# Kernel optimization log

Measured on AMD Instinct MI355X. Metric: run time of the kernel, lower is better.

The kernel has to match this reference:

```python
import jax, jax.numpy as jnp
import numpy as np

B, V = 2048, 64          # batch of polygons, vertices per polygon
D = 2 * V                # data_dim (flattened 2D coords)
HID, TDIM, NL = 256, 128, 4
NH_HID, FPH = 4, 64      # hidden heads, per-head features (hidden_dim//4)
NIN = 2 + 4 + TDIM       # coords + pos_enc(4) + time emb


def _gat_layer(h, src, tgt, W, a_src, a_tgt, b, skip, concat, act, N):
    # gordicaleksa pytorch-GAT GATLayer (imp3), dropout=0
    NH, FOUT = a_src.shape
    proj = (h @ W).reshape(N, NH, FOUT)                       # (N,NH,FOUT)
    s_src = (proj * a_src).sum(-1)                            # (N,NH)
    s_tgt = (proj * a_tgt).sum(-1)
    e = jax.nn.leaky_relu(s_src[src] + s_tgt[tgt], negative_slope=0.2)  # (E,NH)
    m = jax.ops.segment_max(e, tgt, num_segments=N)           # stable segment softmax
    ex = jnp.exp(e - m[tgt])
    denom = jax.ops.segment_sum(ex, tgt, num_segments=N)
    alpha = ex / (denom[tgt] + 1e-16)                         # (E,NH)
    out = jax.ops.segment_sum(proj[src] * alpha[:, :, None], tgt, num_segments=N)
    if skip is None:                                          # FIN == FOUT -> direct residual
        out = out + h[:, None, :]
    else:
        out = out + (h @ skip).reshape(N, NH, FOUT)
    out = out.reshape(N, NH * FOUT) if concat else out.mean(axis=1)
    out = out + b
    return jax.nn.elu(out) if act else out


def _forward(x, t, tW, tb, layers, h1W, h1b, h2W, h2b):
    Bsz, Dd = x.shape
    Vn = Dd // 2
    N = Bsz * Vn
    coords = x.reshape(N, 2)
    graph_index = jnp.repeat(jnp.arange(Bsz), Vn)
    node_index = jnp.tile(jnp.arange(Vn), Bsz)
    # SinusoidalPosEmb(TDIM) + Linear + SiLU
    half = TDIM // 2
    freqs = jnp.exp(-jnp.log(10000.0) * jnp.arange(half, dtype=jnp.float32) / (half - 1))
    te = t.astype(jnp.float32)[:, None] * freqs[None, :]
    temb = jnp.concatenate([jnp.sin(te), jnp.cos(te)], axis=1)
    temb = jax.nn.silu(temb @ tW + tb)
    # cycle positional features
    phase = node_index.astype(jnp.float32) * (2.0 * jnp.pi / Vn)
    pos = jnp.stack([jnp.sin(phase), jnp.cos(phase), jnp.sin(2.0 * phase), jnp.cos(2.0 * phase)], axis=1)
    h = jnp.concatenate([coords, pos, temb[graph_index]], axis=1)  # (N, NIN)
    # cycle edge_index: src=[self,self,self], tgt=[next,prev,self]
    base = graph_index * Vn
    slf = jnp.arange(N)
    nxt = base + jnp.remainder(node_index + 1, Vn)
    prv = base + jnp.remainder(node_index - 1, Vn)
    src = jnp.concatenate([slf, slf, slf])
    tgt = jnp.concatenate([nxt, prv, slf])
    for i, (W, a_s, a_t, b, skip) in enumerate(layers):
        last = (i == len(layers) - 1)
        h = _gat_layer(h, src, tgt, W, a_s, a_t, b, skip, concat=not last, act=not last, N=N)
    h = jax.nn.silu(h @ h1W + h1b)
    noise = h @ h2W + h2b                                     # (N, 2)
    return noise.reshape(Bsz, Dd)


def setup_inputs() -> dict:
    key = jax.random.key(0)
    ks = iter(jax.random.split(key, 48))
    def nrm(shape, s=0.05):
        return (jax.random.normal(next(ks), shape, jnp.float32) * s)
    inp = {}
    inp["x"] = jax.random.normal(next(ks), (B, D), jnp.float32)
    inp["t"] = jax.random.randint(next(ks), (B,), 0, 1000)
    inp["tW"] = nrm((TDIM, TDIM)); inp["tb"] = jnp.zeros((TDIM,), jnp.float32)
    fins = [NIN, NH_HID * FPH, NH_HID * FPH, NH_HID * FPH]
    fouts = [FPH, FPH, FPH, HID]
    nhs = [NH_HID, NH_HID, NH_HID, 1]
    for i in range(NL):
        inp[f"W{i}"] = nrm((fins[i], nhs[i] * fouts[i]))
        inp[f"asrc{i}"] = nrm((nhs[i], fouts[i]))
        inp[f"atgt{i}"] = nrm((nhs[i], fouts[i]))
        inp[f"b{i}"] = jnp.zeros((nhs[i] * fouts[i] if i < NL - 1 else fouts[i],), jnp.float32)
    for i in range(NL - 1):  # last layer: FIN==FOUT -> identity skip
        inp[f"skip{i}"] = nrm((fins[i], nhs[i] * fouts[i]))
    inp["h1W"] = nrm((HID, HID)); inp["h1b"] = jnp.zeros((HID,), jnp.float32)
    inp["h2W"] = nrm((HID, 2)); inp["h2b"] = jnp.zeros((2,), jnp.float32)
    return inp


def reference(x, t, tW, tb,
              W0, asrc0, atgt0, b0, skip0,
              W1, asrc1, atgt1, b1, skip1,
              W2, asrc2, atgt2, b2, skip2,
              W3, asrc3, atgt3, b3,
              h1W, h1b, h2W, h2b):
    layers = [(W0, asrc0, atgt0, b0, skip0),
              (W1, asrc1, atgt1, b1, skip1),
              (W2, asrc2, atgt2, b2, skip2),
              (W3, asrc3, atgt3, b3, None)]
    return _forward(x, t, tW, tb, layers, h1W, h1b, h2W, h2b)
```

## Files before the change

### kernel.cpp

```cpp
#include <hip/hip_runtime.h>
#include <hip/hip_bf16.h>

#define VN    64
#define KPAD  264

typedef __bf16 bf16x8 __attribute__((ext_vector_type(8)));
typedef float  f32x4  __attribute__((ext_vector_type(4)));

#define OFF_W0   0
#define OFF_SK0  40960
#define OFF_W1   81920
#define OFF_SK1  147456
#define OFF_W2   212992
#define OFF_SK2  278528
#define OFF_W3   344064
#define OFF_H1W  409600
#define OFF_END  475136

__global__ void pack_all(const float* __restrict__ W0s, const float* __restrict__ sk0s,
                         const float* __restrict__ W1s, const float* __restrict__ sk1s,
                         const float* __restrict__ W2s, const float* __restrict__ sk2s,
                         const float* __restrict__ W3s, const float* __restrict__ h1Ws,
                         const float* __restrict__ h2W, float* __restrict__ h2wt,
                         __bf16* __restrict__ wp)
{
  int blk = blockIdx.x;
  if (blk >= 1856) {
    int idx = (blk - 1856) * 256 + threadIdx.x;
    int c = idx >> 8, k = idx & 255;
    h2wt[idx] = h2W[k * 2 + c];
    return;
  }
  const float* src; int fin, dstoff, rel;
  if (blk < 320) {
    if (blk < 160) { src = W0s;  dstoff = OFF_W0;  rel = blk; }
    else           { src = sk0s; dstoff = OFF_SK0; rel = blk - 160; }
    fin = 134;
  } else {
    int r = (blk - 320) >> 8;
    rel = (blk - 320) & 255;
    const float* srcs[6] = {W1s, sk1s, W2s, sk2s, W3s, h1Ws};
    const int    offs[6] = {OFF_W1, OFF_SK1, OFF_W2, OFF_SK2, OFF_W3, OFF_H1W};
    src = srcs[r]; dstoff = offs[r]; fin = 256;
  }
  int idx = rel * 256 + threadIdx.x;
  int rr = idx & 7, n = (idx >> 3) & 255, c = idx >> 11;
  int k = c * 8 + rr;
  float v = (k < fin) ? src[k * 256 + n] : 0.0f;
  wp[dstoff + idx] = (__bf16)v;
}

__global__ void temb_kernel(const int* __restrict__ t, const float* __restrict__ tW,
                            const float* __restrict__ tb, float* __restrict__ d_temb)
{
  __shared__ float se[128];
  int b = blockIdx.x, tid = threadIdx.x;
  int fi = tid & 63;
  float fr = expf(-logf(10000.0f) * (float)fi / 63.0f);
  float te = (float)t[b] * fr;
  se[tid] = (tid < 64) ? sinf(te) : cosf(te);
  __syncthreads();
  float a = tb[tid];
  for (int k = 0; k < 128; k++)
    a = fmaf(se[k], tW[k * 128 + tid], a);
  d_temb[b * 128 + tid] = a / (1.0f + expf(-a));
}

template<int KS>
__device__ __forceinline__ void mfma_mm(const __bf16* __restrict__ Bp,
                                        f32x4 acc[4][4],
                                        const __bf16* __restrict__ shA,
                                        int l, int q, int colbase8)
{
#pragma unroll
  for (int s = 0; s < KS; s++) {
    bf16x8 af[4], bfr[4];
#pragma unroll
    for (int rt = 0; rt < 4; rt++)
      af[rt] = *(const bf16x8*)(shA + (rt * 16 + l) * KPAD + s * 32 + q * 8);
#pragma unroll
    for (int ct = 0; ct < 4; ct++)
      bfr[ct] = *(const bf16x8*)(Bp + (s * 4 + q) * 2048 + colbase8 + ct * 128);
#pragma unroll
    for (int rt = 0; rt < 4; rt++)
#pragma unroll
      for (int ct = 0; ct < 4; ct++)
        acc[rt][ct] = __builtin_amdgcn_mfma_f32_16x16x32_bf16(af[rt], bfr[ct], acc[rt][ct], 0, 0, 0);
  }
}

template<int KS>
__device__ __forceinline__ void mfma_dual(const __bf16* __restrict__ Bw,
                                          const __bf16* __restrict__ Bk,
                                          f32x4 accW[4][4], f32x4 accK[4][4],
                                          const __bf16* __restrict__ shA,
                                          int l, int q, int colbase8)
{
#pragma unroll
  for (int s = 0; s < KS; s++) {
    bf16x8 af[4], bw[4], bk[4];
#pragma unroll
    for (int rt = 0; rt < 4; rt++)
      af[rt] = *(const bf16x8*)(shA + (rt * 16 + l) * KPAD + s * 32 + q * 8);
#pragma unroll
    for (int ct = 0; ct < 4; ct++) {
      bw[ct] = *(const bf16x8*)(Bw + (s * 4 + q) * 2048 + colbase8 + ct * 128);
      bk[ct] = *(const bf16x8*)(Bk + (s * 4 + q) * 2048 + colbase8 + ct * 128);
    }
#pragma unroll
    for (int rt = 0; rt < 4; rt++)
#pragma unroll
      for (int ct = 0; ct < 4; ct++) {
        accW[rt][ct] = __builtin_amdgcn_mfma_f32_16x16x32_bf16(af[rt], bw[ct], accW[rt][ct], 0, 0, 0);
        accK[rt][ct] = __builtin_amdgcn_mfma_f32_16x16x32_bf16(af[rt], bk[ct], accK[rt][ct], 0, 0, 0);
      }
  }
}

__global__ __launch_bounds__(256, 2)
void gat_poly_kernel(const float* __restrict__ x,
                     const float* __restrict__ as0, const float* __restrict__ at0, const float* __restrict__ b0,
                     const float* __restrict__ as1, const float* __restrict__ at1, const float* __restrict__ b1,
                     const float* __restrict__ as2, const float* __restrict__ at2, const float* __restrict__ b2,
                     const float* __restrict__ as3, const float* __restrict__ at3, const float* __restrict__ b3,
                     const float* __restrict__ h1b, const float* __restrict__ h2b,
                     const __bf16* __restrict__ WP,
                     const float* __restrict__ h2wt,
                     const float* __restrict__ d_temb,
                     float* __restrict__ out)
{
  __shared__ __bf16 sh_hb[VN * KPAD];
  __shared__ float  sh_temb[128];
  __shared__ float  sh_ssp[VN * 4];
  __shared__ float  sh_stp[VN * 4];
  __shared__ float  sh_al[VN][3];

  const int b    = blockIdx.x;
  const int tid  = threadIdx.x;
  const int w    = tid >> 6;
  const int lane = tid & 63;
  const int l    = lane & 15;
  const int q    = lane >> 4;
  const int cb   = w * 64;
  const int colbase8 = (cb + l) * 8;
  const int lup  = (lane + 16) & 63;
  const int ldn  = (lane + 48) & 63;

  if (tid < 128) sh_temb[tid] = d_temb[b * 128 + tid];
  __syncthreads();

  for (int idx = tid; idx < VN * 160; idx += 256) {
    int n = idx / 160, k = idx - n * 160;
    float v = 0.0f;
    if (k < 2) {
      v = x[b * 128 + 2 * n + k];
    } else if (k < 6) {
      float ph  = (float)n * 0.09817477042468103f;
      float arg = (k < 4) ? ph : 2.0f * ph;
      v = ((k & 1) == 0) ? sinf(arg) : cosf(arg);
    } else if (k < 134) {
      v = sh_temb[k - 6];
    }
    sh_hb[n * KPAD + k] = (__bf16)v;
  }
  __syncthreads();

  const int WOFFS[3]  = {OFF_W0, OFF_W1, OFF_W2};
  const int SOFFS[3]  = {OFF_SK0, OFF_SK1, OFF_SK2};
  const float* Asr[3] = {as0, as1, as2};
  const float* Atg[3] = {at0, at1, at2};
  const float* Bs[3]  = {b0, b1, b2};

  for (int li = 0; li < 3; li++) {
    f32x4 accP[4][4], accS[4][4];
#pragma unroll
    for (int rt = 0; rt < 4; rt++)
#pragma unroll
      for (int ct = 0; ct < 4; ct++) { accP[rt][ct] = (f32x4)0.0f; accS[rt][ct] = (f32x4)0.0f; }

    if (li == 0) mfma_dual<5>(WP + OFF_W0,   WP + OFF_SK0,   accP, accS, sh_hb, l, q, colbase8);
    else         mfma_dual<8>(WP + WOFFS[li], WP + SOFFS[li], accP, accS, sh_hb, l, q, colbase8);

    float ca[4], ta[4];
#pragma unroll
    for (int ct = 0; ct < 4; ct++) {
      ca[ct] = Asr[li][cb + ct * 16 + l];
      ta[ct] = Atg[li][cb + ct * 16 + l];
    }
    float ssA[4][4], stA[4][4];
#pragma unroll
    for (int rt = 0; rt < 4; rt++)
#pragma unroll
      for (int reg = 0; reg < 4; reg++) {
        float ss = accP[rt][0][reg] * ca[0] + accP[rt][1][reg] * ca[1]
                 + accP[rt][2][reg] * ca[2] + accP[rt][3][reg] * ca[3];
        float st = accP[rt][0][reg] * ta[0] + accP[rt][1][reg] * ta[1]
                 + accP[rt][2][reg] * ta[2] + accP[rt][3][reg] * ta[3];
#pragma unroll
        for (int m = 8; m >= 1; m >>= 1) {
          ss += __shfl_xor(ss, m, 64);
          st += __shfl_xor(st, m, 64);
        }
        ssA[rt][reg] = ss;
        stA[rt][reg] = st;
      }

    float al0[4][4], al1[4][4], al2[4][4];
    {
      float s0s[4], s3s[4];
#pragma unroll
      for (int rt = 0; rt < 4; rt++) {
        s0s[rt] = __shfl(ssA[rt][0], lup, 64);
        s3s[rt] = __shfl(ssA[rt][3], ldn, 64);
      }
#pragma unroll
      for (int rt = 0; rt < 4; rt++)
#pragma unroll
        for (int reg = 0; reg < 4; reg++) {
          float ssp = (reg > 0) ? ssA[rt][reg - 1] : ((q > 0) ? s3s[rt] : s3s[(rt + 3) & 3]);
          float ssx = (reg < 3) ? ssA[rt][reg + 1] : ((q < 3) ? s0s[rt] : s0s[(rt + 1) & 3]);
          float stg = stA[rt][reg];
          float e0 = ssp + stg;          e0 = (e0 < 0.0f) ? 0.2f * e0 : e0;
          float e1 = ssx + stg;          e1 = (e1 < 0.0f) ? 0.2f * e1 : e1;
          float e2 = ssA[rt][reg] + stg; e2 = (e2 < 0.0f) ? 0.2f * e2 : e2;
          float mx = fmaxf(e0, fmaxf(e1, e2));
          float x0 = expf(e0 - mx), x1 = expf(e1 - mx), x2 = expf(e2 - mx);
          float inv = 1.0f / (x0 + x1 + x2 + 1e-16f);
          al0[rt][reg] = x0 * inv;
          al1[rt][reg] = x1 * inv;
          al2[rt][reg] = x2 * inv;
        }
    }

    __syncthreads();

    {
      float b4[4];
#pragma unroll
      for (int ct = 0; ct < 4; ct++) b4[ct] = Bs[li][cb + ct * 16 + l];
#pragma unroll
      for (int ct = 0; ct < 4; ct++) {
        float p0s[4], p3s[4];
#pragma unroll
        for (int rt = 0; rt < 4; rt++) {
          p0s[rt] = __shfl(accP[rt][ct][0], lup, 64);
          p3s[rt] = __shfl(accP[rt][ct][3], ldn, 64);
        }
#pragma unroll
        for (int rt = 0; rt < 4; rt++)
#pragma unroll
          for (int reg = 0; reg < 4; reg++) {
            float pv = (reg > 0) ? accP[rt][ct][reg - 1] : ((q > 0) ? p3s[rt] : p3s[(rt + 3) & 3]);
            float nx = (reg < 3) ? accP[rt][ct][reg + 1] : ((q < 3) ? p0s[rt] : p0s[(rt + 1) & 3]);
            float o = accS[rt][ct][reg]
                    + al0[rt][reg] * pv + al1[rt][reg] * nx
                    + al2[rt][reg] * accP[rt][ct][reg] + b4[ct];
            o = (o > 0.0f) ? o : (expf(o) - 1.0f);
            sh_hb[(rt * 16 + q * 4 + reg) * KPAD + cb + ct * 16 + l] = (__bf16)o;
          }
      }
    }
    __syncthreads();
  }

  {
    f32x4 accP[4][4];
#pragma unroll
    for (int rt = 0; rt < 4; rt++)
#pragma unroll
      for (int ct = 0; ct < 4; ct++) accP[rt][ct] = (f32x4)0.0f;
    mfma_mm<8>(WP + OFF_W3, accP, sh_hb, l, q, colbase8);

    {
      float ca[4], ta[4];
#pragma unroll
      for (int ct = 0; ct < 4; ct++) {
        ca[ct] = as3[cb + ct * 16 + l];
        ta[ct] = at3[cb + ct * 16 + l];
      }
#pragma unroll
      for (int rt = 0; rt < 4; rt++)
#pragma unroll
        for (int reg = 0; reg < 4; reg++) {
          float ss = accP[rt][0][reg] * ca[0] + accP[rt][1][reg] * ca[1]
                   + accP[rt][2][reg] * ca[2] + accP[rt][3][reg] * ca[3];
          float st = accP[rt][0][reg] * ta[0] + accP[rt][1][reg] * ta[1]
                   + accP[rt][2][reg] * ta[2] + accP[rt][3][reg] * ta[3];
#pragma unroll
          for (int m = 8; m >= 1; m >>= 1) {
            ss += __shfl_xor(ss, m, 64);
            st += __shfl_xor(st, m, 64);
          }
          if (l == 0) {
            int n = rt * 16 + q * 4 + reg;
            sh_ssp[n * 4 + w] = ss;
            sh_stp[n * 4 + w] = st;
          }
        }
    }
    __syncthreads();

    if (tid < 64) {
      int n = tid;
      float ssn = sh_ssp[n * 4] + sh_ssp[n * 4 + 1] + sh_ssp[n * 4 + 2] + sh_ssp[n * 4 + 3];
      float stn = sh_stp[n * 4] + sh_stp[n * 4 + 1] + sh_stp[n * 4 + 2] + sh_stp[n * 4 + 3];
      float ssp = __shfl(ssn, (n + 63) & 63, 64);
      float ssx = __shfl(ssn, (n + 1) & 63, 64);
      float e0 = ssp + stn; e0 = (e0 < 0.0f) ? 0.2f * e0 : e0;
      float e1 = ssx + stn; e1 = (e1 < 0.0f) ? 0.2f * e1 : e1;
      float e2 = ssn + stn; e2 = (e2 < 0.0f) ? 0.2f * e2 : e2;
      float mx = fmaxf(e0, fmaxf(e1, e2));
      float x0 = expf(e0 - mx), x1 = expf(e1 - mx), x2 = expf(e2 - mx);
      float inv = 1.0f / (x0 + x1 + x2 + 1e-16f);
      sh_al[n][0] = x0 * inv;
      sh_al[n][1] = x1 * inv;
      sh_al[n][2] = x2 * inv;
    }
    __syncthreads();

    {
      float b4[4];
#pragma unroll
      for (int ct = 0; ct < 4; ct++) b4[ct] = b3[cb + ct * 16 + l];
      float a0r[4][4], a1r[4][4], a2r[4][4];
#pragma unroll
      for (int rt = 0; rt < 4; rt++)
#pragma unroll
        for (int reg = 0; reg < 4; reg++) {
          int n = rt * 16 + q * 4 + reg;
          a0r[rt][reg] = sh_al[n][0];
          a1r[rt][reg] = sh_al[n][1];
          a2r[rt][reg] = sh_al[n][2];
        }
#pragma unroll
      for (int ct = 0; ct < 4; ct++) {
        float p0s[4], p3s[4];
#pragma unroll
        for (int rt = 0; rt < 4; rt++) {
          p0s[rt] = __shfl(accP[rt][ct][0], lup, 64);
          p3s[rt] = __shfl(accP[rt][ct][3], ldn, 64);
        }
#pragma unroll
        for (int rt = 0; rt < 4; rt++)
#pragma unroll
          for (int reg = 0; reg < 4; reg++) {
            float pv = (reg > 0) ? accP[rt][ct][reg - 1] : ((q > 0) ? p3s[rt] : p3s[(rt + 3) & 3]);
            float nx = (reg < 3) ? accP[rt][ct][reg + 1] : ((q < 3) ? p0s[rt] : p0s[(rt + 1) & 3]);
            int addr = (rt * 16 + q * 4 + reg) * KPAD + cb + ct * 16 + l;
            float hres = (float)sh_hb[addr];
            float o = a0r[rt][reg] * pv + a1r[rt][reg] * nx
                    + a2r[rt][reg] * accP[rt][ct][reg]
                    + hres + b4[ct];
            sh_hb[addr] = (__bf16)o;
          }
      }
    }
    __syncthreads();
  }

  {
    f32x4 acc[4][4];
#pragma unroll
    for (int rt = 0; rt < 4; rt++)
#pragma unroll
      for (int ct = 0; ct < 4; ct++) acc[rt][ct] = (f32x4)0.0f;
    mfma_mm<8>(WP + OFF_H1W, acc, sh_hb, l, q, colbase8);
    __syncthreads();

    float b4[4];
#pragma unroll
    for (int ct = 0; ct < 4; ct++) b4[ct] = h1b[cb + ct * 16 + l];
#pragma unroll
    for (int rt = 0; rt < 4; rt++)
#pragma unroll
      for (int reg = 0; reg < 4; reg++) {
        int n = rt * 16 + q * 4 + reg;
#pragma unroll
        for (int ct = 0; ct < 4; ct++) {
          float o = acc[rt][ct][reg] + b4[ct];
          o = o / (1.0f + expf(-o));
          sh_hb[n * KPAD + cb + ct * 16 + l] = (__bf16)o;
        }
      }
    __syncthreads();

    {
      int n = tid >> 2, c = (tid >> 1) & 1, half = tid & 1;
      const float* wrow = h2wt + c * 256 + half * 128;
      const __bf16* hrow = sh_hb + n * KPAD + half * 128;
      float o = half ? 0.0f : h2b[c];
#pragma unroll 4
      for (int k8 = 0; k8 < 16; k8++) {
        bf16x8 hv = *(const bf16x8*)(hrow + k8 * 8);
        f32x4 w0 = *(const f32x4*)(wrow + k8 * 8);
        f32x4 w1 = *(const f32x4*)(wrow + k8 * 8 + 4);
#pragma unroll
        for (int j = 0; j < 4; j++) o = fmaf((float)hv[j], w0[j], o);
#pragma unroll
        for (int j = 0; j < 4; j++) o = fmaf((float)hv[4 + j], w1[j], o);
      }
      o += __shfl_xor(o, 1, 64);
      if (!half) out[b * 128 + 2 * n + c] = o;
    }
  }
}

extern "C" void kernel_launch(void* const* d_in, const int* in_sizes, int n_in,
                              void* d_out, int out_size, void* d_ws, size_t ws_size,
                              hipStream_t stream)
{
  auto fp = [&](int i) { return (const float*)d_in[i]; };
  __bf16* wp   = (__bf16*)d_ws;
  float* h2wt  = (float*)(wp + OFF_END);
  float* dtemb = h2wt + 512;

  pack_all<<<1858, 256, 0, stream>>>(fp(4), fp(20), fp(8), fp(21),
                                     fp(12), fp(22), fp(16), fp(23),
                                     fp(25), h2wt, wp);
  temb_kernel<<<2048, 128, 0, stream>>>((const int*)d_in[1], fp(2), fp(3), dtemb);

  gat_poly_kernel<<<2048, 256, 0, stream>>>(
      fp(0),
      fp(5),  fp(6),  fp(7),
      fp(9),  fp(10), fp(11),
      fp(13), fp(14), fp(15),
      fp(17), fp(18), fp(19),
      fp(24), fp(26),
      wp, h2wt, dtemb,
      (float*)d_out);
}
```

Before: 431.9 us.

## Split GAT block across eight waves with half-width column tiles

Doubles the workgroup to 512 threads so each wave computes 32 output columns instead of 64. Per-wave accumulators shrink to 4x2 tiles, which cuts register pressure and allows more waves in flight. Attention scores are now partial per wave, so they are combined through shared memory with extra barriers, and the output head is split four ways. The cost is more synchronisation and more shared-memory traffic, and each wave reloads the full A fragments from LDS for half the MFMA work.

```diff
diff --git a/kernel.cpp b/kernel.cpp
--- a/kernel.cpp
+++ b/kernel.cpp
@@ -68,23 +68,23 @@
 
 template<int KS>
 __device__ __forceinline__ void mfma_mm(const __bf16* __restrict__ Bp,
-                                        f32x4 acc[4][4],
+                                        f32x4 acc[4][2],
                                         const __bf16* __restrict__ shA,
                                         int l, int q, int colbase8)
 {
 #pragma unroll
   for (int s = 0; s < KS; s++) {
-    bf16x8 af[4], bfr[4];
+    bf16x8 af[4], bfr[2];
 #pragma unroll
     for (int rt = 0; rt < 4; rt++)
       af[rt] = *(const bf16x8*)(shA + (rt * 16 + l) * KPAD + s * 32 + q * 8);
 #pragma unroll
-    for (int ct = 0; ct < 4; ct++)
+    for (int ct = 0; ct < 2; ct++)
       bfr[ct] = *(const bf16x8*)(Bp + (s * 4 + q) * 2048 + colbase8 + ct * 128);
 #pragma unroll
     for (int rt = 0; rt < 4; rt++)
 #pragma unroll
-      for (int ct = 0; ct < 4; ct++)
+      for (int ct = 0; ct < 2; ct++)
         acc[rt][ct] = __builtin_amdgcn_mfma_f32_16x16x32_bf16(af[rt], bfr[ct], acc[rt][ct], 0, 0, 0);
   }
 }
@@ -92,32 +92,32 @@
 template<int KS>
 __device__ __forceinline__ void mfma_dual(const __bf16* __restrict__ Bw,
                                           const __bf16* __restrict__ Bk,
-                                          f32x4 accW[4][4], f32x4 accK[4][4],
+                                          f32x4 accW[4][2], f32x4 accK[4][2],
                                           const __bf16* __restrict__ shA,
                                           int l, int q, int colbase8)
 {
 #pragma unroll
   for (int s = 0; s < KS; s++) {
-    bf16x8 af[4], bw[4], bk[4];
+    bf16x8 af[4], bw[2], bk[2];
 #pragma unroll
     for (int rt = 0; rt < 4; rt++)
       af[rt] = *(const bf16x8*)(shA + (rt * 16 + l) * KPAD + s * 32 + q * 8);
 #pragma unroll
-    for (int ct = 0; ct < 4; ct++) {
+    for (int ct = 0; ct < 2; ct++) {
       bw[ct] = *(const bf16x8*)(Bw + (s * 4 + q) * 2048 + colbase8 + ct * 128);
       bk[ct] = *(const bf16x8*)(Bk + (s * 4 + q) * 2048 + colbase8 + ct * 128);
     }
 #pragma unroll
     for (int rt = 0; rt < 4; rt++)
 #pragma unroll
-      for (int ct = 0; ct < 4; ct++) {
+      for (int ct = 0; ct < 2; ct++) {
         accW[rt][ct] = __builtin_amdgcn_mfma_f32_16x16x32_bf16(af[rt], bw[ct], accW[rt][ct], 0, 0, 0);
         accK[rt][ct] = __builtin_amdgcn_mfma_f32_16x16x32_bf16(af[rt], bk[ct], accK[rt][ct], 0, 0, 0);
       }
   }
 }
 
-__global__ __launch_bounds__(256, 2)
+__global__ __launch_bounds__(512, 2)
 void gat_poly_kernel(const float* __restrict__ x,
                      const float* __restrict__ as0, const float* __restrict__ at0, const float* __restrict__ b0,
                      const float* __restrict__ as1, const float* __restrict__ at1, const float* __restrict__ b1,
@@ -131,17 +131,21 @@
 {
   __shared__ __bf16 sh_hb[VN * KPAD];
   __shared__ float  sh_temb[128];
-  __shared__ float  sh_ssp[VN * 4];
-  __shared__ float  sh_stp[VN * 4];
+  __shared__ float  sh_ssp[512];
+  __shared__ float  sh_stp[512];
+  __shared__ float  sh_ssc[256];
+  __shared__ float  sh_stc[256];
   __shared__ float  sh_al[VN][3];
 
   const int b    = blockIdx.x;
   const int tid  = threadIdx.x;
-  const int w    = tid >> 6;
+  const int wid  = tid >> 6;
   const int lane = tid & 63;
   const int l    = lane & 15;
   const int q    = lane >> 4;
-  const int cb   = w * 64;
+  const int w2   = wid >> 1;
+  const int ch   = wid & 1;
+  const int cb   = w2 * 64 + ch * 32;
   const int colbase8 = (cb + l) * 8;
   const int lup  = (lane + 16) & 63;
   const int ldn  = (lane + 48) & 63;
@@ -149,7 +153,7 @@
   if (tid < 128) sh_temb[tid] = d_temb[b * 128 + tid];
   __syncthreads();
 
-  for (int idx = tid; idx < VN * 160; idx += 256) {
+  for (int idx = tid; idx < VN * 160; idx += 512) {
     int n = idx / 160, k = idx - n * 160;
     float v = 0.0f;
     if (k < 2) {
@@ -172,74 +176,73 @@
   const float* Bs[3]  = {b0, b1, b2};
 
   for (int li = 0; li < 3; li++) {
-    f32x4 accP[4][4], accS[4][4];
-#pragma unroll
-    for (int rt = 0; rt < 4; rt++)
-#pragma unroll
-      for (int ct = 0; ct < 4; ct++) { accP[rt][ct] = (f32x4)0.0f; accS[rt][ct] = (f32x4)0.0f; }
+    f32x4 accP[4][2], accS[4][2];
+#pragma unroll
+    for (int rt = 0; rt < 4; rt++)
+#pragma unroll
+      for (int ct = 0; ct < 2; ct++) { accP[rt][ct] = (f32x4)0.0f; accS[rt][ct] = (f32x4)0.0f; }
 
     if (li == 0) mfma_dual<5>(WP + OFF_W0,   WP + OFF_SK0,   accP, accS, sh_hb, l, q, colbase8);
     else         mfma_dual<8>(WP + WOFFS[li], WP + SOFFS[li], accP, accS, sh_hb, l, q, colbase8);
 
-    float ca[4], ta[4];
-#pragma unroll
-    for (int ct = 0; ct < 4; ct++) {
-      ca[ct] = Asr[li][cb + ct * 16 + l];
-      ta[ct] = Atg[li][cb + ct * 16 + l];
-    }
-    float ssA[4][4], stA[4][4];
+    {
+      float ca[2], ta[2];
+#pragma unroll
+      for (int ct = 0; ct < 2; ct++) {
+        ca[ct] = Asr[li][cb + ct * 16 + l];
+        ta[ct] = Atg[li][cb + ct * 16 + l];
+      }
+#pragma unroll
+      for (int rt = 0; rt < 4; rt++)
+#pragma unroll
+        for (int reg = 0; reg < 4; reg++) {
+          float ss = accP[rt][0][reg] * ca[0] + accP[rt][1][reg] * ca[1];
+          float st = accP[rt][0][reg] * ta[0] + accP[rt][1][reg] * ta[1];
+#pragma unroll
+          for (int m = 8; m >= 1; m >>= 1) {
+            ss += __shfl_xor(ss, m, 64);
+            st += __shfl_xor(st, m, 64);
+          }
+          if (l == 0) {
+            int n = rt * 16 + q * 4 + reg;
+            sh_ssp[(w2 * 64 + n) * 2 + ch] = ss;
+            sh_stp[(w2 * 64 + n) * 2 + ch] = st;
+          }
+        }
+    }
+    __syncthreads();
+
+    if (tid < 256) {
+      sh_ssc[tid] = sh_ssp[tid * 2] + sh_ssp[tid * 2 + 1];
+      sh_stc[tid] = sh_stp[tid * 2] + sh_stp[tid * 2 + 1];
+    }
+    __syncthreads();
+
+    float al0[4][4], al1[4][4], al2[4][4];
 #pragma unroll
     for (int rt = 0; rt < 4; rt++)
 #pragma unroll
       for (int reg = 0; reg < 4; reg++) {
-        float ss = accP[rt][0][reg] * ca[0] + accP[rt][1][reg] * ca[1]
-                 + accP[rt][2][reg] * ca[2] + accP[rt][3][reg] * ca[3];
-        float st = accP[rt][0][reg] * ta[0] + accP[rt][1][reg] * ta[1]
-                 + accP[rt][2][reg] * ta[2] + accP[rt][3][reg] * ta[3];
-#pragma unroll
-        for (int m = 8; m >= 1; m >>= 1) {
-          ss += __shfl_xor(ss, m, 64);
-          st += __shfl_xor(st, m, 64);
-        }
-        ssA[rt][reg] = ss;
-        stA[rt][reg] = st;
-      }
-
-    float al0[4][4], al1[4][4], al2[4][4];
+        int n = rt * 16 + q * 4 + reg;
+        int prv = (n + 63) & 63, nxt = (n + 1) & 63;
+        float stn = sh_stc[w2 * 64 + n];
+        float e0 = sh_ssc[w2 * 64 + prv] + stn; e0 = (e0 < 0.0f) ? 0.2f * e0 : e0;
+        float e1 = sh_ssc[w2 * 64 + nxt] + stn; e1 = (e1 < 0.0f) ? 0.2f * e1 : e1;
+        float e2 = sh_ssc[w2 * 64 + n]   + stn; e2 = (e2 < 0.0f) ? 0.2f * e2 : e2;
+        float mx = fmaxf(e0, fmaxf(e1, e2));
+        float x0 = expf(e0 - mx), x1 = expf(e1 - mx), x2 = expf(e2 - mx);
+        float inv = 1.0f / (x0 + x1 + x2 + 1e-16f);
+        al0[rt][reg] = x0 * inv;
+        al1[rt][reg] = x1 * inv;
+        al2[rt][reg] = x2 * inv;
+      }
+
     {
-      float s0s[4], s3s[4];
-#pragma unroll
-      for (int rt = 0; rt < 4; rt++) {
-        s0s[rt] = __shfl(ssA[rt][0], lup, 64);
-        s3s[rt] = __shfl(ssA[rt][3], ldn, 64);
-      }
-#pragma unroll
-      for (int rt = 0; rt < 4; rt++)
-#pragma unroll
-        for (int reg = 0; reg < 4; reg++) {
-          float ssp = (reg > 0) ? ssA[rt][reg - 1] : ((q > 0) ? s3s[rt] : s3s[(rt + 3) & 3]);
-          float ssx = (reg < 3) ? ssA[rt][reg + 1] : ((q < 3) ? s0s[rt] : s0s[(rt + 1) & 3]);
-          float stg = stA[rt][reg];
-          float e0 = ssp + stg;          e0 = (e0 < 0.0f) ? 0.2f * e0 : e0;
-          float e1 = ssx + stg;          e1 = (e1 < 0.0f) ? 0.2f * e1 : e1;
-          float e2 = ssA[rt][reg] + stg; e2 = (e2 < 0.0f) ? 0.2f * e2 : e2;
-          float mx = fmaxf(e0, fmaxf(e1, e2));
-          float x0 = expf(e0 - mx), x1 = expf(e1 - mx), x2 = expf(e2 - mx);
-          float inv = 1.0f / (x0 + x1 + x2 + 1e-16f);
-          al0[rt][reg] = x0 * inv;
-          al1[rt][reg] = x1 * inv;
-          al2[rt][reg] = x2 * inv;
-        }
-    }
-
-    __syncthreads();
-
-    {
-      float b4[4];
-#pragma unroll
-      for (int ct = 0; ct < 4; ct++) b4[ct] = Bs[li][cb + ct * 16 + l];
-#pragma unroll
-      for (int ct = 0; ct < 4; ct++) {
+      float b2r[2];
+#pragma unroll
+      for (int ct = 0; ct < 2; ct++) b2r[ct] = Bs[li][cb + ct * 16 + l];
+#pragma unroll
+      for (int ct = 0; ct < 2; ct++) {
         float p0s[4], p3s[4];
 #pragma unroll
         for (int rt = 0; rt < 4; rt++) {
@@ -254,7 +257,7 @@
             float nx = (reg < 3) ? accP[rt][ct][reg + 1] : ((q < 3) ? p0s[rt] : p0s[(rt + 1) & 3]);
             float o = accS[rt][ct][reg]
                     + al0[rt][reg] * pv + al1[rt][reg] * nx
-                    + al2[rt][reg] * accP[rt][ct][reg] + b4[ct];
+                    + al2[rt][reg] * accP[rt][ct][reg] + b2r[ct];
             o = (o > 0.0f) ? o : (expf(o) - 1.0f);
             sh_hb[(rt * 16 + q * 4 + reg) * KPAD + cb + ct * 16 + l] = (__bf16)o;
           }
@@ -264,17 +267,17 @@
   }
 
   {
-    f32x4 accP[4][4];
-#pragma unroll
-    for (int rt = 0; rt < 4; rt++)
-#pragma unroll
-      for (int ct = 0; ct < 4; ct++) accP[rt][ct] = (f32x4)0.0f;
+    f32x4 accP[4][2];
+#pragma unroll
+    for (int rt = 0; rt < 4; rt++)
+#pragma unroll
+      for (int ct = 0; ct < 2; ct++) accP[rt][ct] = (f32x4)0.0f;
     mfma_mm<8>(WP + OFF_W3, accP, sh_hb, l, q, colbase8);
 
     {
-      float ca[4], ta[4];
-#pragma unroll
-      for (int ct = 0; ct < 4; ct++) {
+      float ca[2], ta[2];
+#pragma unroll
+      for (int ct = 0; ct < 2; ct++) {
         ca[ct] = as3[cb + ct * 16 + l];
         ta[ct] = at3[cb + ct * 16 + l];
       }
@@ -282,10 +285,8 @@
       for (int rt = 0; rt < 4; rt++)
 #pragma unroll
         for (int reg = 0; reg < 4; reg++) {
-          float ss = accP[rt][0][reg] * ca[0] + accP[rt][1][reg] * ca[1]
-                   + accP[rt][2][reg] * ca[2] + accP[rt][3][reg] * ca[3];
-          float st = accP[rt][0][reg] * ta[0] + accP[rt][1][reg] * ta[1]
-                   + accP[rt][2][reg] * ta[2] + accP[rt][3][reg] * ta[3];
+          float ss = accP[rt][0][reg] * ca[0] + accP[rt][1][reg] * ca[1];
+          float st = accP[rt][0][reg] * ta[0] + accP[rt][1][reg] * ta[1];
 #pragma unroll
           for (int m = 8; m >= 1; m >>= 1) {
             ss += __shfl_xor(ss, m, 64);
@@ -293,8 +294,8 @@
           }
           if (l == 0) {
             int n = rt * 16 + q * 4 + reg;
-            sh_ssp[n * 4 + w] = ss;
-            sh_stp[n * 4 + w] = st;
+            sh_ssp[n * 8 + wid] = ss;
+            sh_stp[n * 8 + wid] = st;
           }
         }
     }
@@ -302,8 +303,9 @@
 
     if (tid < 64) {
       int n = tid;
-      float ssn = sh_ssp[n * 4] + sh_ssp[n * 4 + 1] + sh_ssp[n * 4 + 2] + sh_ssp[n * 4 + 3];
-      float stn = sh_stp[n * 4] + sh_stp[n * 4 + 1] + sh_stp[n * 4 + 2] + sh_stp[n * 4 + 3];
+      float ssn = 0.0f, stn = 0.0f;
+#pragma unroll
+      for (int k = 0; k < 8; k++) { ssn += sh_ssp[n * 8 + k]; stn += sh_stp[n * 8 + k]; }
       float ssp = __shfl(ssn, (n + 63) & 63, 64);
       float ssx = __shfl(ssn, (n + 1) & 63, 64);
       float e0 = ssp + stn; e0 = (e0 < 0.0f) ? 0.2f * e0 : e0;
@@ -319,9 +321,9 @@
     __syncthreads();
 
     {
-      float b4[4];
-#pragma unroll
-      for (int ct = 0; ct < 4; ct++) b4[ct] = b3[cb + ct * 16 + l];
+      float b2r[2];
+#pragma unroll
+      for (int ct = 0; ct < 2; ct++) b2r[ct] = b3[cb + ct * 16 + l];
       float a0r[4][4], a1r[4][4], a2r[4][4];
 #pragma unroll
       for (int rt = 0; rt < 4; rt++)
@@ -333,7 +335,7 @@
           a2r[rt][reg] = sh_al[n][2];
         }
 #pragma unroll
-      for (int ct = 0; ct < 4; ct++) {
+      for (int ct = 0; ct < 2; ct++) {
         float p0s[4], p3s[4];
 #pragma unroll
         for (int rt = 0; rt < 4; rt++) {
@@ -350,7 +352,7 @@
             float hres = (float)sh_hb[addr];
             float o = a0r[rt][reg] * pv + a1r[rt][reg] * nx
                     + a2r[rt][reg] * accP[rt][ct][reg]
-                    + hres + b4[ct];
+                    + hres + b2r[ct];
             sh_hb[addr] = (__bf16)o;
           }
       }
@@ -359,25 +361,25 @@
   }
 
   {
-    f32x4 acc[4][4];
-#pragma unroll
-    for (int rt = 0; rt < 4; rt++)
-#pragma unroll
-      for (int ct = 0; ct < 4; ct++) acc[rt][ct] = (f32x4)0.0f;
+    f32x4 acc[4][2];
+#pragma unroll
+    for (int rt = 0; rt < 4; rt++)
+#pragma unroll
+      for (int ct = 0; ct < 2; ct++) acc[rt][ct] = (f32x4)0.0f;
     mfma_mm<8>(WP + OFF_H1W, acc, sh_hb, l, q, colbase8);
     __syncthreads();
 
-    float b4[4];
-#pragma unroll
-    for (int ct = 0; ct < 4; ct++) b4[ct] = h1b[cb + ct * 16 + l];
+    float b2r[2];
+#pragma unroll
+    for (int ct = 0; ct < 2; ct++) b2r[ct] = h1b[cb + ct * 16 + l];
 #pragma unroll
     for (int rt = 0; rt < 4; rt++)
 #pragma unroll
       for (int reg = 0; reg < 4; reg++) {
         int n = rt * 16 + q * 4 + reg;
 #pragma unroll
-        for (int ct = 0; ct < 4; ct++) {
-          float o = acc[rt][ct][reg] + b4[ct];
+        for (int ct = 0; ct < 2; ct++) {
+          float o = acc[rt][ct][reg] + b2r[ct];
           o = o / (1.0f + expf(-o));
           sh_hb[n * KPAD + cb + ct * 16 + l] = (__bf16)o;
         }
@@ -385,12 +387,12 @@
     __syncthreads();
 
     {
-      int n = tid >> 2, c = (tid >> 1) & 1, half = tid & 1;
-      const float* wrow = h2wt + c * 256 + half * 128;
-      const __bf16* hrow = sh_hb + n * KPAD + half * 128;
-      float o = half ? 0.0f : h2b[c];
-#pragma unroll 4
-      for (int k8 = 0; k8 < 16; k8++) {
+      int n = tid >> 3, c = (tid >> 2) & 1, qtr = tid & 3;
+      const float* wrow = h2wt + c * 256 + qtr * 64;
+      const __bf16* hrow = sh_hb + n * KPAD + qtr * 64;
+      float o = (qtr == 0) ? h2b[c] : 0.0f;
+#pragma unroll
+      for (int k8 = 0; k8 < 8; k8++) {
         bf16x8 hv = *(const bf16x8*)(hrow + k8 * 8);
         f32x4 w0 = *(const f32x4*)(wrow + k8 * 8);
         f32x4 w1 = *(const f32x4*)(wrow + k8 * 8 + 4);
@@ -400,7 +402,8 @@
         for (int j = 0; j < 4; j++) o = fmaf((float)hv[4 + j], w1[j], o);
       }
       o += __shfl_xor(o, 1, 64);
-      if (!half) out[b * 128 + 2 * n + c] = o;
+      o += __shfl_xor(o, 2, 64);
+      if (qtr == 0) out[b * 128 + 2 * n + c] = o;
     }
   }
 }
@@ -419,7 +422,7 @@
                                      fp(25), h2wt, wp);
   temb_kernel<<<2048, 128, 0, stream>>>((const int*)d_in[1], fp(2), fp(3), dtemb);
 
-  gat_poly_kernel<<<2048, 256, 0, stream>>>(
+  gat_poly_kernel<<<2048, 512, 0, stream>>>(
       fp(0),
       fp(5),  fp(6),  fp(7),
       fp(9),  fp(10), fp(11),
```

Result: slower. 575.8 us (+33.3%).
